# Kernel optimization log

Hardware: AMD Instinct MI355X
Metric: run time of the kernel (lower is better)

## Reference

```python
import jax, jax.numpy as jnp
import numpy as np

B, L, H = 4, 256, 768  # batch, seq_len, hidden_size


def setup_inputs() -> dict:
    key = jax.random.key(0)
    k1, k2 = jax.random.split(key, 2)
    seq_hiddens = jax.random.normal(k1, (B, L, H), dtype=jnp.float32)
    # combine_fc: Linear(2*H -> H)
    W = jax.random.normal(k2, (H, 2 * H), dtype=jnp.float32) * 0.02
    b = jnp.zeros((H,), dtype=jnp.float32)
    return {"seq_hiddens": seq_hiddens, "W": W, "b": b}


def reference(seq_hiddens, W, b):
    # Vectorized handshaking ('cat' type): for each pair (i, j) with j >= i,
    # out[p] = tanh(Linear(concat(h_i, h_j))). Pair order matches the torch
    # loop: i ascending, then j ascending (row-major upper triangle).
    L_ = seq_hiddens.shape[1]
    ii, jj = np.triu_indices(L_)          # static index arrays, P = L(L+1)/2
    rep = seq_hiddens[:, ii, :]           # (B, P, H) h_i repeated
    vis = seq_hiddens[:, jj, :]           # (B, P, H) visible suffix hiddens
    x = jnp.concatenate([rep, vis], axis=-1)   # (B, P, 2H)
    out = jnp.tanh(jnp.einsum('bpk,hk->bph', x, W) + b)  # (B, P, H)
    return out
```

## Files before the change

### kernel.cpp

```cpp
#include <hip/hip_runtime.h>
#include <hip/hip_bf16.h>
#include <math.h>

#define B_ 4
#define L_ 256
#define H_ 768
#define P_ 32896
#define N_ 1536
#define K_ 768
#define M_ 1024

typedef __attribute__((ext_vector_type(4))) float f32x4;
typedef __attribute__((ext_vector_type(8))) short s16x8;
typedef const __attribute__((address_space(1))) void* gptr_t;
typedef __attribute__((address_space(3))) void* sptr_t;

__device__ __forceinline__ unsigned pack_bf16(float x, float y) {
    __hip_bfloat16 hx = __float2bfloat16(x);
    __hip_bfloat16 hy = __float2bfloat16(y);
    const unsigned short ux = *(const unsigned short*)&hx;
    const unsigned short uy = *(const unsigned short*)&hy;
    return (unsigned)ux | ((unsigned)uy << 16);
}

__global__ __launch_bounds__(256) void convert_to_bf16(
        const float* __restrict__ A, const float* __restrict__ W,
        unsigned short* __restrict__ Abf, unsigned short* __restrict__ Wbf) {
    const int idx = blockIdx.x * 256 + threadIdx.x;
    const int nA4 = (M_ * K_) / 4;
    const int nW4 = (H_ * N_) / 4;
    if (idx < nA4) {
        const float4 v = ((const float4*)A)[idx];
        ((uint2*)Abf)[idx] = make_uint2(pack_bf16(v.x, v.y), pack_bf16(v.z, v.w));
    } else if (idx < nA4 + nW4) {
        const int wi = idx - nA4;
        const int h  = wi / 384;
        const int c  = (wi % 384) * 4;
        const float4 v = ((const float4*)W)[wi];
        const int n = h + ((c >= 768) ? 768 : 0);
        const int k = (c >= 768) ? (c - 768) : c;
        *(uint2*)(Wbf + (size_t)n * K_ + k) =
            make_uint2(pack_bf16(v.x, v.y), pack_bf16(v.z, v.w));
    }
}

__global__ __launch_bounds__(256) void gemm_uv_bf16(
        const unsigned short* __restrict__ Abf,
        const unsigned short* __restrict__ Wbf,
        const float* __restrict__ bias, float* __restrict__ T) {
    __shared__ __align__(16) char As[2][64 * 128];
    __shared__ __align__(16) char Bs[2][64 * 128];

    const int tid  = threadIdx.x;
    const int bm   = blockIdx.x * 64;
    const int bn   = blockIdx.y * 64;
    const int lane = tid & 63;
    const int wave = tid >> 6;

    const int wm  = (wave & 1) * 32;
    const int wn  = (wave >> 1) * 32;
    const int l15 = lane & 15;
    const int l4  = lane >> 4;

    const int rl = lane >> 3;
    const int cc = lane & 7;
    const int srow0 = wave * 16;
    const int r0 = srow0 + rl;
    const int r1 = srow0 + 8 + rl;
    const int cp0 = cc ^ (r0 & 7);
    const int cp1 = cc ^ (r1 & 7);
    const unsigned short* a0p = Abf + (size_t)(bm + r0) * K_ + cp0 * 8;
    const unsigned short* a1p = Abf + (size_t)(bm + r1) * K_ + cp1 * 8;
    const unsigned short* w0p = Wbf + (size_t)(bn + r0) * K_ + cp0 * 8;
    const unsigned short* w1p = Wbf + (size_t)(bn + r1) * K_ + cp1 * 8;

    f32x4 acc[2][2] = {};

#define STAGE(bb, kt)                                                        \
    do {                                                                     \
        __builtin_amdgcn_global_load_lds((gptr_t)(a0p + (kt)),               \
            (sptr_t)(As[bb] + srow0 * 128), 16, 0, 0);                       \
        __builtin_amdgcn_global_load_lds((gptr_t)(w0p + (kt)),               \
            (sptr_t)(Bs[bb] + srow0 * 128), 16, 0, 0);                       \
        __builtin_amdgcn_global_load_lds((gptr_t)(a1p + (kt)),               \
            (sptr_t)(As[bb] + (srow0 + 8) * 128), 16, 0, 0);                 \
        __builtin_amdgcn_global_load_lds((gptr_t)(w1p + (kt)),               \
            (sptr_t)(Bs[bb] + (srow0 + 8) * 128), 16, 0, 0);                 \
    } while (0)

    STAGE(0, 0);
    __syncthreads();

    for (int t = 0; t < 12; ++t) {
        const int cur = t & 1;
        if (t + 1 < 12) STAGE(cur ^ 1, (t + 1) * 64);

        const char* pA = As[cur];
        const char* pB = Bs[cur];
#pragma unroll
        for (int ks = 0; ks < 2; ++ks) {
            s16x8 af[2], bf[2];
#pragma unroll
            for (int mi = 0; mi < 2; ++mi) {
                const int row = wm + mi * 16 + l15;
                const int chunk = (ks * 4 + l4) ^ (row & 7);
                af[mi] = *(const s16x8*)(pA + row * 128 + chunk * 16);
            }
#pragma unroll
            for (int ni = 0; ni < 2; ++ni) {
                const int row = wn + ni * 16 + l15;
                const int chunk = (ks * 4 + l4) ^ (row & 7);
                bf[ni] = *(const s16x8*)(pB + row * 128 + chunk * 16);
            }
#pragma unroll
            for (int mi = 0; mi < 2; ++mi)
#pragma unroll
                for (int ni = 0; ni < 2; ++ni)
                    acc[mi][ni] = __builtin_amdgcn_mfma_f32_16x16x32_bf16(
                        af[mi], bf[ni], acc[mi][ni], 0, 0, 0);
        }
        __syncthreads();
    }
#undef STAGE

#pragma unroll
    for (int mi = 0; mi < 2; ++mi)
#pragma unroll
        for (int ni = 0; ni < 2; ++ni) {
            const int gm0 = bm + wm + mi * 16 + l4 * 4;
            const int gn  = bn + wn + ni * 16 + l15;
            const float badd = (gn < H_) ? bias[gn] : 0.0f;
#pragma unroll
            for (int r = 0; r < 4; ++r)
                T[(size_t)(gm0 + r) * N_ + gn] = acc[mi][ni][r] + badd;
        }
}

__global__ __launch_bounds__(256) void gemm_uv_mfma(
        const float* __restrict__ A, const float* __restrict__ W,
        const float* __restrict__ bias, float* __restrict__ T) {
    __shared__ __align__(16) char As[64 * 128];
    __shared__ __align__(16) char Bs[64 * 128];

    const int tid = threadIdx.x;
    const int bm = blockIdx.x * 64;
    const int bn = blockIdx.y * 64;
    const int lane = tid & 63;
    const int wave = tid >> 6;

    const int sr = tid >> 4;
    const int sk = (tid & 15) * 4;
    const float* wbase = (bn < H_) ? (W + (size_t)bn * N_)
                                   : (W + (size_t)(bn - H_) * N_ + H_);

    const int wm = (wave & 1) * 32;
    const int wn = (wave >> 1) * 32;
    const int l15 = lane & 15;
    const int l4  = lane >> 4;

    f32x4 acc[2][2] = {};

    for (int kt = 0; kt < K_; kt += 64) {
        __syncthreads();
#pragma unroll
        for (int ph = 0; ph < 4; ++ph) {
            const int row = ph * 16 + sr;
            const float4 av = *(const float4*)(A + (size_t)(bm + row) * K_ + kt + sk);
            const float4 bv = *(const float4*)(wbase + (size_t)row * N_ + kt + sk);
            const int chunk = sk >> 3;
            const int sub   = (sk & 4) ? 8 : 0;
            const int boff  = row * 128 + ((chunk ^ (row & 7)) * 16) + sub;
            *(uint2*)(As + boff) = make_uint2(pack_bf16(av.x, av.y), pack_bf16(av.z, av.w));
            *(uint2*)(Bs + boff) = make_uint2(pack_bf16(bv.x, bv.y), pack_bf16(bv.z, bv.w));
        }
        __syncthreads();
#pragma unroll
        for (int ks = 0; ks < 2; ++ks) {
            s16x8 af[2], bf[2];
#pragma unroll
            for (int mi = 0; mi < 2; ++mi) {
                const int row = wm + mi * 16 + l15;
                const int chunk = (ks * 4 + l4) ^ (row & 7);
                af[mi] = *(const s16x8*)(As + row * 128 + chunk * 16);
            }
#pragma unroll
            for (int ni = 0; ni < 2; ++ni) {
                const int row = wn + ni * 16 + l15;
                const int chunk = (ks * 4 + l4) ^ (row & 7);
                bf[ni] = *(const s16x8*)(Bs + row * 128 + chunk * 16);
            }
#pragma unroll
            for (int mi = 0; mi < 2; ++mi)
#pragma unroll
                for (int ni = 0; ni < 2; ++ni)
                    acc[mi][ni] = __builtin_amdgcn_mfma_f32_16x16x32_bf16(
                        af[mi], bf[ni], acc[mi][ni], 0, 0, 0);
        }
    }

#pragma unroll
    for (int mi = 0; mi < 2; ++mi)
#pragma unroll
        for (int ni = 0; ni < 2; ++ni) {
            const int gm0 = bm + wm + mi * 16 + l4 * 4;
            const int gn  = bn + wn + ni * 16 + l15;
            const float badd = (gn < H_) ? bias[gn] : 0.0f;
#pragma unroll
            for (int r = 0; r < 4; ++r)
                T[(size_t)(gm0 + r) * N_ + gn] = acc[mi][ni][r] + badd;
        }
}

__device__ __forceinline__ float fast_tanh(float x) {
    const float e = __builtin_amdgcn_exp2f(x * 2.885390081777926815f);
    const float r = __builtin_amdgcn_rcpf(e + 1.0f);
    return fmaf(-2.0f, r, 1.0f);
}

__device__ __forceinline__ f32x4 tanh4(f32x4 u, f32x4 v) {
    f32x4 o;
    o.x = fast_tanh(u.x + v.x);
    o.y = fast_tanh(u.y + v.y);
    o.z = fast_tanh(u.z + v.z);
    o.w = fast_tanh(u.w + v.w);
    return o;
}

#define NROWS_ (B_ * P_)
#define NQUAD_ (NROWS_ / 4)
#define EGRID_ 1024

__global__ __launch_bounds__(192) void handshake_epilogue_quad(
        const float* __restrict__ T,
        float* __restrict__ out) {
    const int h = threadIdx.x * 4;

    for (int q = blockIdx.x; q < NQUAD_; q += EGRID_) {
        const int rbase = q * 4;
        const int b  = rbase / P_;
        const int p0 = rbase - b * P_;

        const float Df = (float)(263169 - 8 * p0);
        int i = (int)((513.0f - __builtin_sqrtf(Df)) * 0.5f);
        if ((i + 1) * (513 - (i + 1)) / 2 <= p0) ++i;
        if (i * (513 - i) / 2 > p0) --i;
        int j = p0 - i * (513 - i) / 2 + i;

        const float* Tb = T + (size_t)b * L_ * N_;
        f32x4 u = *(const f32x4*)(Tb + (size_t)i * N_ + h);
        float* orow = out + (size_t)rbase * H_ + h;

#pragma unroll
        for (int k = 0; k < 4; ++k) {
            const f32x4 v = *(const f32x4*)(Tb + (size_t)j * N_ + H_ + h);
            __builtin_nontemporal_store(tanh4(u, v), (f32x4*)orow);
            orow += H_;
            ++j;
            if (j == 256) {
                ++i; j = i;
                u = *(const f32x4*)(Tb + (size_t)i * N_ + h);
            }
        }
    }
}

extern "C" void kernel_launch(void* const* d_in, const int* in_sizes, int n_in,
                              void* d_out, int out_size, void* d_ws, size_t ws_size,
                              hipStream_t stream) {
    const float* seq  = (const float*)d_in[0];
    const float* W    = (const float*)d_in[1];
    const float* bias = (const float*)d_in[2];
    float* out = (float*)d_out;

    char* ws = (char*)d_ws;
    float* T = (float*)ws;
    const size_t T_BYTES = (size_t)M_ * N_ * 4;
    unsigned short* Abf = (unsigned short*)(ws + T_BYTES);
    unsigned short* Wbf = (unsigned short*)(ws + T_BYTES + (size_t)M_ * K_ * 2);
    const size_t NEED = T_BYTES + (size_t)M_ * K_ * 2 + (size_t)K_ * N_ * 2;

    dim3 g1(M_ / 64, N_ / 64);
    if (ws_size >= NEED) {
        convert_to_bf16<<<1920, 256, 0, stream>>>(seq, W, Abf, Wbf);
        gemm_uv_bf16<<<g1, 256, 0, stream>>>(Abf, Wbf, bias, T);
    } else {
        gemm_uv_mfma<<<g1, 256, 0, stream>>>(seq, W, bias, T);
    }

    handshake_epilogue_quad<<<EGRID_, 192, 0, stream>>>(T, out);
}
```

Before: 93.55 us.

## Split GEMM K dimension in two and reduce partials in epilogue

The bf16 GEMM now takes a z grid dimension that splits the 12 K-steps across two blocks. Each block writes its partial product to a separate T buffer, and bias is added only by the first split. A new epilogue kernel sums the two partial buffers while applying tanh to each pair. This doubles GEMM parallelism on a small grid, at the cost of extra workspace and twice the T reads in the epilogue.

```diff
diff --git a/kernel.cpp b/kernel.cpp
--- a/kernel.cpp
+++ b/kernel.cpp
@@ -54,9 +54,13 @@
     const int tid  = threadIdx.x;
     const int bm   = blockIdx.x * 64;
     const int bn   = blockIdx.y * 64;
+    const int kz   = blockIdx.z;
+    const int nst  = 12 / gridDim.z;
+    const int koff = kz * nst * 64;
+    float* Tout = T + (size_t)kz * M_ * N_;
+
     const int lane = tid & 63;
     const int wave = tid >> 6;
-
     const int wm  = (wave & 1) * 32;
     const int wn  = (wave >> 1) * 32;
     const int l15 = lane & 15;
@@ -69,10 +73,10 @@
     const int r1 = srow0 + 8 + rl;
     const int cp0 = cc ^ (r0 & 7);
     const int cp1 = cc ^ (r1 & 7);
-    const unsigned short* a0p = Abf + (size_t)(bm + r0) * K_ + cp0 * 8;
-    const unsigned short* a1p = Abf + (size_t)(bm + r1) * K_ + cp1 * 8;
-    const unsigned short* w0p = Wbf + (size_t)(bn + r0) * K_ + cp0 * 8;
-    const unsigned short* w1p = Wbf + (size_t)(bn + r1) * K_ + cp1 * 8;
+    const unsigned short* a0p = Abf + (size_t)(bm + r0) * K_ + koff + cp0 * 8;
+    const unsigned short* a1p = Abf + (size_t)(bm + r1) * K_ + koff + cp1 * 8;
+    const unsigned short* w0p = Wbf + (size_t)(bn + r0) * K_ + koff + cp0 * 8;
+    const unsigned short* w1p = Wbf + (size_t)(bn + r1) * K_ + koff + cp1 * 8;
 
     f32x4 acc[2][2] = {};
 
@@ -91,9 +95,9 @@
     STAGE(0, 0);
     __syncthreads();
 
-    for (int t = 0; t < 12; ++t) {
+    for (int t = 0; t < nst; ++t) {
         const int cur = t & 1;
-        if (t + 1 < 12) STAGE(cur ^ 1, (t + 1) * 64);
+        if (t + 1 < nst) STAGE(cur ^ 1, (t + 1) * 64);
 
         const char* pA = As[cur];
         const char* pB = Bs[cur];
@@ -129,10 +133,10 @@
         for (int ni = 0; ni < 2; ++ni) {
             const int gm0 = bm + wm + mi * 16 + l4 * 4;
             const int gn  = bn + wn + ni * 16 + l15;
-            const float badd = (gn < H_) ? bias[gn] : 0.0f;
+            const float badd = (kz == 0 && gn < H_) ? bias[gn] : 0.0f;
 #pragma unroll
             for (int r = 0; r < 4; ++r)
-                T[(size_t)(gm0 + r) * N_ + gn] = acc[mi][ni][r] + badd;
+                Tout[(size_t)(gm0 + r) * N_ + gn] = acc[mi][ni][r] + badd;
         }
 }
 
@@ -230,6 +234,44 @@
 #define NQUAD_ (NROWS_ / 4)
 #define EGRID_ 1024
 
+__global__ __launch_bounds__(192) void handshake_epilogue_quad2(
+        const float* __restrict__ T,
+        float* __restrict__ out) {
+    const int h = threadIdx.x * 4;
+    const float* __restrict__ T1 = T + (size_t)M_ * N_;
+
+    for (int q = blockIdx.x; q < NQUAD_; q += EGRID_) {
+        const int rbase = q * 4;
+        const int b  = rbase / P_;
+        const int p0 = rbase - b * P_;
+
+        const float Df = (float)(263169 - 8 * p0);
+        int i = (int)((513.0f - __builtin_sqrtf(Df)) * 0.5f);
+        if ((i + 1) * (513 - (i + 1)) / 2 <= p0) ++i;
+        if (i * (513 - i) / 2 > p0) --i;
+        int j = p0 - i * (513 - i) / 2 + i;
+
+        const size_t tb = (size_t)b * L_ * N_;
+        f32x4 u = *(const f32x4*)(T + tb + (size_t)i * N_ + h)
+                + *(const f32x4*)(T1 + tb + (size_t)i * N_ + h);
+        float* orow = out + (size_t)rbase * H_ + h;
+
+#pragma unroll
+        for (int k = 0; k < 4; ++k) {
+            const f32x4 v = *(const f32x4*)(T + tb + (size_t)j * N_ + H_ + h)
+                          + *(const f32x4*)(T1 + tb + (size_t)j * N_ + H_ + h);
+            __builtin_nontemporal_store(tanh4(u, v), (f32x4*)orow);
+            orow += H_;
+            ++j;
+            if (j == 256) {
+                ++i; j = i;
+                u = *(const f32x4*)(T + tb + (size_t)i * N_ + h)
+                  + *(const f32x4*)(T1 + tb + (size_t)i * N_ + h);
+            }
+        }
+    }
+}
+
 __global__ __launch_bounds__(192) void handshake_epilogue_quad(
         const float* __restrict__ T,
         float* __restrict__ out) {
@@ -275,17 +317,28 @@
     char* ws = (char*)d_ws;
     float* T = (float*)ws;
     const size_t T_BYTES = (size_t)M_ * N_ * 4;
-    unsigned short* Abf = (unsigned short*)(ws + T_BYTES);
-    unsigned short* Wbf = (unsigned short*)(ws + T_BYTES + (size_t)M_ * K_ * 2);
-    const size_t NEED = T_BYTES + (size_t)M_ * K_ * 2 + (size_t)K_ * N_ * 2;
-
-    dim3 g1(M_ / 64, N_ / 64);
-    if (ws_size >= NEED) {
+    const size_t AB_BYTES = (size_t)M_ * K_ * 2;
+    const size_t WB_BYTES = (size_t)K_ * N_ * 2;
+    const size_t NEED2 = 2 * T_BYTES + AB_BYTES + WB_BYTES;
+    const size_t NEED1 = T_BYTES + AB_BYTES + WB_BYTES;
+
+    if (ws_size >= NEED2) {
+        unsigned short* Abf = (unsigned short*)(ws + 2 * T_BYTES);
+        unsigned short* Wbf = (unsigned short*)(ws + 2 * T_BYTES + AB_BYTES);
         convert_to_bf16<<<1920, 256, 0, stream>>>(seq, W, Abf, Wbf);
+        dim3 g1(M_ / 64, N_ / 64, 2);
         gemm_uv_bf16<<<g1, 256, 0, stream>>>(Abf, Wbf, bias, T);
+        handshake_epilogue_quad2<<<EGRID_, 192, 0, stream>>>(T, out);
+    } else if (ws_size >= NEED1) {
+        unsigned short* Abf = (unsigned short*)(ws + T_BYTES);
+        unsigned short* Wbf = (unsigned short*)(ws + T_BYTES + AB_BYTES);
+        convert_to_bf16<<<1920, 256, 0, stream>>>(seq, W, Abf, Wbf);
+        dim3 g1(M_ / 64, N_ / 64, 1);
+        gemm_uv_bf16<<<g1, 256, 0, stream>>>(Abf, Wbf, bias, T);
+        handshake_epilogue_quad<<<EGRID_, 192, 0, stream>>>(T, out);
     } else {
+        dim3 g1(M_ / 64, N_ / 64);
         gemm_uv_mfma<<<g1, 256, 0, stream>>>(seq, W, bias, T);
-    }
-
-    handshake_epilogue_quad<<<EGRID_, 192, 0, stream>>>(T, out);
-}
+        handshake_epilogue_quad<<<EGRID_, 192, 0, stream>>>(T, out);
+    }
+}
```

Measured after the change: 90.81 us, median of 2. -2.9%, faster.
